# Kernel optimization log

Hardware: AMD Instinct MI355X
Metric: run time of the kernel (lower is better)

Reference implementation:

```python
import jax, jax.numpy as jnp
import numpy as np

N_COL, N_CON, E = 100000, 20000, 800000
D_COL, D_CON, H = 16, 8, 128


def _segment_mean(msgs, dst_idx, n_dst):
    # sum then divide by in-degree (0-degree nodes get 0, matching PyG scatter-mean)
    s = jax.ops.segment_sum(msgs, dst_idx, num_segments=n_dst)
    cnt = jax.ops.segment_sum(jnp.ones((dst_idx.shape[0], 1), msgs.dtype), dst_idx, num_segments=n_dst)
    return s / jnp.maximum(cnt, 1.0)


def _sage(x_src, x_dst, src_idx, dst_idx, Wl, bl, Wr):
    # PyG SAGEConv(mean): lin_l(mean_j x_j) + lin_r(x_i); lin_r has no bias
    agg = _segment_mean(x_src[src_idx], dst_idx, x_dst.shape[0])
    return agg @ Wl.T + bl + x_dst @ Wr.T


def setup_inputs():
    key = jax.random.key(0)
    ks = jax.random.split(key, 24)
    rn = lambda k, shape, s=0.05: jax.random.normal(k, shape, jnp.float32) * s
    z = lambda shape: jnp.zeros(shape, jnp.float32)
    inp = {
        'x_col': jax.random.normal(ks[0], (N_COL, D_COL), jnp.float32),
        'x_con': jax.random.normal(ks[1], (N_CON, D_CON), jnp.float32),
        'edge_col': jax.random.randint(ks[2], (E,), 0, N_COL, jnp.int32),
        'edge_con': jax.random.randint(ks[3], (E,), 0, N_CON, jnp.int32),
        'W_col': rn(ks[4], (H, D_COL)), 'b_col': z((H,)),
        'W_con': rn(ks[5], (H, D_CON)), 'b_con': z((H,)),
        'c1_cn_Wl': rn(ks[6], (H, H)), 'c1_cn_bl': z((H,)), 'c1_cn_Wr': rn(ks[7], (H, H)),
        'c1_nc_Wl': rn(ks[8], (H, H)), 'c1_nc_bl': z((H,)), 'c1_nc_Wr': rn(ks[9], (H, H)),
        'c2_cn_Wl': rn(ks[10], (H, H)), 'c2_cn_bl': z((H,)), 'c2_cn_Wr': rn(ks[11], (H, H)),
        'c2_nc_Wl': rn(ks[12], (H, H)), 'c2_nc_bl': z((H,)), 'c2_nc_Wr': rn(ks[13], (H, H)),
        'q_W1': rn(ks[14], (H // 2, H)), 'q_b1': z((H // 2,)),
        'q_W2': rn(ks[15], (1, H // 2)), 'q_b2': z((1,)),
    }
    return inp


def reference(x_col, x_con, edge_col, edge_con,
              W_col, b_col, W_con, b_con,
              c1_cn_Wl, c1_cn_bl, c1_cn_Wr, c1_nc_Wl, c1_nc_bl, c1_nc_Wr,
              c2_cn_Wl, c2_cn_bl, c2_cn_Wr, c2_nc_Wl, c2_nc_bl, c2_nc_Wr,
              q_W1, q_b1, q_W2, q_b2):
    relu = jax.nn.relu
    h_col = relu(x_col @ W_col.T + b_col)  # [N_COL, H]
    h_con = relu(x_con @ W_con.T + b_con)  # [N_CON, H]
    # conv1: 'serves' col->con, 'served_by' con->col (reverse edges)
    n_con = relu(_sage(h_col, h_con, edge_col, edge_con, c1_cn_Wl, c1_cn_bl, c1_cn_Wr))
    n_col = relu(_sage(h_con, h_col, edge_con, edge_col, c1_nc_Wl, c1_nc_bl, c1_nc_Wr))
    # conv2
    h_con2 = relu(_sage(n_col, n_con, edge_col, edge_con, c2_cn_Wl, c2_cn_bl, c2_cn_Wr))
    h_col2 = relu(_sage(n_con, n_col, edge_con, edge_col, c2_nc_Wl, c2_nc_bl, c2_nc_Wr))
    del h_con2  # constraint embeddings unused for Q-head
    q = relu(h_col2 @ q_W1.T + q_b1) @ q_W2.T + q_b2  # [N_COL, 1]
    return q[:, 0]
```

## Files before the change

### kernel.cpp

```cpp
#include <hip/hip_runtime.h>

#define N_COL 100000
#define N_CON 20000
#define HDIM 128
#define SCAN_B 1024

__global__ void transpose_k(const float* __restrict__ src, float* __restrict__ dst, int R, int C) {
    int idx = blockIdx.x * blockDim.x + threadIdx.x;
    if (idx < R * C) {
        int r = idx / C, c = idx - r * C;
        dst[c * R + r] = src[idx];
    }
}

template <int D>
__global__ __launch_bounds__(256) void encoder_k(const float* __restrict__ x,
                                                 const float* __restrict__ WT,
                                                 const float* __restrict__ b,
                                                 float* __restrict__ out, int N) {
    int idx = blockIdx.x * blockDim.x + threadIdx.x;
    if (idx >= N * HDIM) return;
    int n = idx >> 7, h = idx & 127;
    const float* xr = x + (size_t)n * D;
    float acc = b[h];
#pragma unroll
    for (int k = 0; k < D; k++) acc = fmaf(xr[k], WT[k * HDIM + h], acc);
    out[idx] = fmaxf(acc, 0.f);
}

__global__ void count_k(const int* __restrict__ ecol, const int* __restrict__ econ,
                        int* cnt_col, int* cnt_con, int E) {
    int e = blockIdx.x * blockDim.x + threadIdx.x;
    if (e < E) {
        atomicAdd(&cnt_col[ecol[e]], 1);
        atomicAdd(&cnt_con[econ[e]], 1);
    }
}

__global__ __launch_bounds__(256) void scan1_k(const int* __restrict__ cnt, int n,
                                               int* __restrict__ offs, int* __restrict__ partials) {
    __shared__ int lds[256];
    int t = threadIdx.x;
    int base = blockIdx.x * SCAN_B + t * 4;
    int v[4], s = 0;
#pragma unroll
    for (int i = 0; i < 4; i++) { int idx = base + i; v[i] = (idx < n) ? cnt[idx] : 0; s += v[i]; }
    lds[t] = s; __syncthreads();
    for (int off = 1; off < 256; off <<= 1) {
        int x = (t >= off) ? lds[t - off] : 0; __syncthreads();
        lds[t] += x; __syncthreads();
    }
    int excl = lds[t] - s;
    if (t == 255) partials[blockIdx.x] = lds[255];
    int run = excl;
#pragma unroll
    for (int i = 0; i < 4; i++) { int idx = base + i; if (idx < n) offs[idx] = run; run += v[i]; }
}

__global__ __launch_bounds__(256) void scan2_k(int* partials, int nb) {
    __shared__ int lds[256];
    int t = threadIdx.x;
    int v = (t < nb) ? partials[t] : 0;
    lds[t] = v; __syncthreads();
    for (int off = 1; off < 256; off <<= 1) {
        int x = (t >= off) ? lds[t - off] : 0; __syncthreads();
        lds[t] += x; __syncthreads();
    }
    if (t < nb) partials[t] = lds[t] - v;
}

__global__ void scan3_k(int* offs, int n, const int* __restrict__ partials) {
    int i = blockIdx.x * blockDim.x + threadIdx.x;
    if (i < n) offs[i] += partials[i / SCAN_B];
}

__global__ void fill_k(const int* __restrict__ sidx, const int* __restrict__ didx,
                       const int* __restrict__ offs, int* cursor, int* __restrict__ srclist, int E) {
    int e = blockIdx.x * blockDim.x + threadIdx.x;
    if (e < E) {
        int d = didx[e];
        int p = offs[d] + atomicAdd(&cursor[d], 1);
        srclist[p] = sidx[e];
    }
}

__global__ __launch_bounds__(256) void gather_mean_k(const float* __restrict__ tab,
                                                     const int* __restrict__ srclist,
                                                     const int* __restrict__ offs,
                                                     const int* __restrict__ cnt,
                                                     float* __restrict__ out, int N) {
    int wid = threadIdx.x >> 6, lane = threadIdx.x & 63;
    int n = blockIdx.x * 4 + wid;
    if (n >= N) return;
    int c = cnt[n], st = offs[n];
    const int* sl = srclist + st;
    int half = lane >> 5, q = (lane & 31) * 4;
    float ax = 0.f, ay = 0.f, az = 0.f, aw = 0.f;
    int j = 0;
    for (; j + 1 < c; j += 2) {
        int s = sl[j + half];
        float4 a = *reinterpret_cast<const float4*>(tab + (size_t)s * HDIM + q);
        ax += a.x; ay += a.y; az += a.z; aw += a.w;
    }
    if (j < c && half == 0) {
        int s = sl[j];
        float4 a = *reinterpret_cast<const float4*>(tab + (size_t)s * HDIM + q);
        ax += a.x; ay += a.y; az += a.z; aw += a.w;
    }
    ax += __shfl_xor(ax, 32); ay += __shfl_xor(ay, 32);
    az += __shfl_xor(az, 32); aw += __shfl_xor(aw, 32);
    if (half == 0) {
        float inv = 1.f / fmaxf((float)c, 1.f);
        float4 r; r.x = ax * inv; r.y = ay * inv; r.z = az * inv; r.w = aw * inv;
        *reinterpret_cast<float4*>(out + (size_t)n * HDIM + q) = r;
    }
}

__global__ __launch_bounds__(256) void gather_dual_k(const float* __restrict__ t1,
                                                     const float* __restrict__ t2,
                                                     const int* __restrict__ srclist,
                                                     const int* __restrict__ offs,
                                                     const int* __restrict__ cnt,
                                                     float* __restrict__ o1,
                                                     float* __restrict__ o2, int N) {
    int wid = threadIdx.x >> 6, lane = threadIdx.x & 63;
    int n = blockIdx.x * 4 + wid;
    if (n >= N) return;
    int c = cnt[n], st = offs[n];
    const int* sl = srclist + st;
    int half = lane >> 5, q = (lane & 31) * 4;
    const float* tab = half ? t2 : t1;
    float ax = 0.f, ay = 0.f, az = 0.f, aw = 0.f;
    int j = 0;
    for (; j + 1 < c; j += 2) {
        int s0 = sl[j], s1 = sl[j + 1];
        float4 a = *reinterpret_cast<const float4*>(tab + (size_t)s0 * HDIM + q);
        float4 b = *reinterpret_cast<const float4*>(tab + (size_t)s1 * HDIM + q);
        ax += a.x + b.x; ay += a.y + b.y; az += a.z + b.z; aw += a.w + b.w;
    }
    if (j < c) {
        int s0 = sl[j];
        float4 a = *reinterpret_cast<const float4*>(tab + (size_t)s0 * HDIM + q);
        ax += a.x; ay += a.y; az += a.z; aw += a.w;
    }
    float inv = 1.f / fmaxf((float)c, 1.f);
    float4 r; r.x = ax * inv; r.y = ay * inv; r.z = az * inv; r.w = aw * inv;
    float* op = (half ? o2 : o1) + (size_t)n * HDIM + q;
    *reinterpret_cast<float4*>(op) = r;
}

__device__ __forceinline__ void gemm_core(float (*As)[36], float (*Ws)[132],
                                          const float* __restrict__ src,
                                          const float* __restrict__ W,
                                          int n0, int N, int t, float acc[4][8]) {
    int tx = t & 15, ty = t >> 4;
    int ar = t >> 2, akq = (t & 3) * 8;
    int wk = t >> 3, wc = (t & 7) * 16;
    for (int kb = 0; kb < 4; ++kb) {
        int k0 = kb * 32;
        {
            int row = n0 + ar;
            float4 v0 = make_float4(0.f, 0.f, 0.f, 0.f), v1 = v0;
            if (row < N) {
                const float* ap = src + (size_t)row * HDIM + k0 + akq;
                v0 = *reinterpret_cast<const float4*>(ap);
                v1 = *reinterpret_cast<const float4*>(ap + 4);
            }
            *reinterpret_cast<float4*>(&As[ar][akq]) = v0;
            *reinterpret_cast<float4*>(&As[ar][akq + 4]) = v1;
        }
        {
            const float* wp = W + (size_t)(k0 + wk) * HDIM + wc;
#pragma unroll
            for (int jj = 0; jj < 4; jj++)
                *reinterpret_cast<float4*>(&Ws[wk][wc + 4 * jj]) =
                    *reinterpret_cast<const float4*>(wp + 4 * jj);
        }
        __syncthreads();
#pragma unroll
        for (int k4 = 0; k4 < 8; ++k4) {
            float4 av[4];
#pragma unroll
            for (int i = 0; i < 4; i++)
                av[i] = *reinterpret_cast<const float4*>(&As[ty * 4 + i][k4 * 4]);
#pragma unroll
            for (int kk = 0; kk < 4; kk++) {
                float4 w0 = *reinterpret_cast<const float4*>(&Ws[k4 * 4 + kk][tx * 4]);
                float4 w1 = *reinterpret_cast<const float4*>(&Ws[k4 * 4 + kk][64 + tx * 4]);
                float w[8] = {w0.x, w0.y, w0.z, w0.w, w1.x, w1.y, w1.z, w1.w};
#pragma unroll
                for (int i = 0; i < 4; i++) {
                    float avk = (kk == 0) ? av[i].x : (kk == 1) ? av[i].y
                                : (kk == 2) ? av[i].z : av[i].w;
#pragma unroll
                    for (int j = 0; j < 8; j++) acc[i][j] = fmaf(avk, w[j], acc[i][j]);
                }
            }
        }
        __syncthreads();
    }
}

__device__ __forceinline__ void gemm_core_h(float (*Ha)[132], float (*Ws)[132],
                                            const float* __restrict__ W,
                                            int t, float acc[4][8]) {
    int tx = t & 15, ty = t >> 4;
    int wk = t >> 3, wc = (t & 7) * 16;
    for (int kb = 0; kb < 4; ++kb) {
        int k0 = kb * 32;
        {
            const float* wp = W + (size_t)(k0 + wk) * HDIM + wc;
#pragma unroll
            for (int jj = 0; jj < 4; jj++)
                *reinterpret_cast<float4*>(&Ws[wk][wc + 4 * jj]) =
                    *reinterpret_cast<const float4*>(wp + 4 * jj);
        }
        __syncthreads();
#pragma unroll
        for (int k4 = 0; k4 < 8; ++k4) {
            float4 av[4];
#pragma unroll
            for (int i = 0; i < 4; i++)
                av[i] = *reinterpret_cast<const float4*>(&Ha[ty * 4 + i][k0 + k4 * 4]);
#pragma unroll
            for (int kk = 0; kk < 4; kk++) {
                float4 w0 = *reinterpret_cast<const float4*>(&Ws[k4 * 4 + kk][tx * 4]);
                float4 w1 = *reinterpret_cast<const float4*>(&Ws[k4 * 4 + kk][64 + tx * 4]);
                float w[8] = {w0.x, w0.y, w0.z, w0.w, w1.x, w1.y, w1.z, w1.w};
#pragma unroll
                for (int i = 0; i < 4; i++) {
                    float avk = (kk == 0) ? av[i].x : (kk == 1) ? av[i].y
                                : (kk == 2) ? av[i].z : av[i].w;
#pragma unroll
                    for (int j = 0; j < 8; j++) acc[i][j] = fmaf(avk, w[j], acc[i][j]);
                }
            }
        }
        __syncthreads();
    }
}

__global__ __launch_bounds__(256) void lin_k(const float* __restrict__ src,
                                             const float* __restrict__ WT,
                                             float* __restrict__ out, int N) {
    __shared__ __align__(16) float As[64][36];
    __shared__ __align__(16) float Ws[32][132];
    int t = threadIdx.x;
    int tx = t & 15, ty = t >> 4;
    int n0 = blockIdx.x * 64;
    float acc[4][8];
#pragma unroll
    for (int i = 0; i < 4; i++)
#pragma unroll
        for (int j = 0; j < 8; j++) acc[i][j] = 0.f;
    gemm_core(As, Ws, src, WT, n0, N, t, acc);
#pragma unroll
    for (int i = 0; i < 4; i++) {
        int row = n0 + ty * 4 + i;
        if (row < N) {
            float* op = out + (size_t)row * HDIM;
            *reinterpret_cast<float4*>(op + tx * 4) = make_float4(acc[i][0], acc[i][1], acc[i][2], acc[i][3]);
            *reinterpret_cast<float4*>(op + 64 + tx * 4) = make_float4(acc[i][4], acc[i][5], acc[i][6], acc[i][7]);
        }
    }
}

__global__ __launch_bounds__(256) void sage_gemm_k(const float* __restrict__ agg,
                                                   const float* __restrict__ xdst,
                                                   const float* __restrict__ WlT,
                                                   const float* __restrict__ bl,
                                                   const float* __restrict__ WrT,
                                                   float* __restrict__ out, int N) {
    __shared__ __align__(16) float As[64][36];
    __shared__ __align__(16) float Ws[32][132];
    int t = threadIdx.x;
    int tx = t & 15, ty = t >> 4;
    int n0 = blockIdx.x * 64;
    float acc[4][8];
#pragma unroll
    for (int i = 0; i < 4; i++)
#pragma unroll
        for (int j = 0; j < 8; j++) acc[i][j] = 0.f;
    gemm_core(As, Ws, agg, WlT, n0, N, t, acc);
    gemm_core(As, Ws, xdst, WrT, n0, N, t, acc);
    float4 b0 = *reinterpret_cast<const float4*>(bl + tx * 4);
    float4 b1 = *reinterpret_cast<const float4*>(bl + 64 + tx * 4);
    float bb[8] = {b0.x, b0.y, b0.z, b0.w, b1.x, b1.y, b1.z, b1.w};
#pragma unroll
    for (int i = 0; i < 4; i++) {
        int row = n0 + ty * 4 + i;
        if (row < N) {
            float4 r0, r1;
            r0.x = fmaxf(acc[i][0] + bb[0], 0.f);
            r0.y = fmaxf(acc[i][1] + bb[1], 0.f);
            r0.z = fmaxf(acc[i][2] + bb[2], 0.f);
            r0.w = fmaxf(acc[i][3] + bb[3], 0.f);
            r1.x = fmaxf(acc[i][4] + bb[4], 0.f);
            r1.y = fmaxf(acc[i][5] + bb[5], 0.f);
            r1.z = fmaxf(acc[i][6] + bb[6], 0.f);
            r1.w = fmaxf(acc[i][7] + bb[7], 0.f);
            float* op = out + (size_t)row * HDIM;
            *reinterpret_cast<float4*>(op + tx * 4) = r0;
            *reinterpret_cast<float4*>(op + 64 + tx * 4) = r1;
        }
    }
}

__global__ __launch_bounds__(256) void col_mega_k(const float* __restrict__ c0_1,
                                                  const float* __restrict__ c0_2,
                                                  const float* __restrict__ xdst,
                                                  const float* __restrict__ Wr1T,
                                                  const float* __restrict__ bl1,
                                                  const float* __restrict__ Wr2T,
                                                  const float* __restrict__ bl2,
                                                  const float* __restrict__ W1T,
                                                  const float* __restrict__ b1v,
                                                  const float* __restrict__ W2,
                                                  const float* __restrict__ b2,
                                                  float* __restrict__ out, int N) {
    __shared__ __align__(16) char smem[50688];
    float (*H)[132] = reinterpret_cast<float(*)[132]>(smem);
    float (*Ws)[132] = reinterpret_cast<float(*)[132]>(smem + 33792);
    int t = threadIdx.x;
    int tx = t & 15, ty = t >> 4;
    int n0 = blockIdx.x * 64;

    {
        int xr = t >> 2, xc0 = (t & 3) * 32;
        int row = n0 + xr;
        if (row < N) {
            const float* xp = xdst + (size_t)row * HDIM + xc0;
#pragma unroll
            for (int jj = 0; jj < 8; jj++)
                *reinterpret_cast<float4*>(&H[xr][xc0 + 4 * jj]) =
                    *reinterpret_cast<const float4*>(xp + 4 * jj);
        } else {
            float4 z = make_float4(0.f, 0.f, 0.f, 0.f);
#pragma unroll
            for (int jj = 0; jj < 8; jj++)
                *reinterpret_cast<float4*>(&H[xr][xc0 + 4 * jj]) = z;
        }
    }
    float acc[4][8];
#pragma unroll
    for (int i = 0; i < 4; i++)
#pragma unroll
        for (int j = 0; j < 8; j++) acc[i][j] = 0.f;
    gemm_core_h(H, Ws, Wr1T, t, acc);
    {
        float4 b0 = *reinterpret_cast<const float4*>(bl1 + tx * 4);
        float4 b1 = *reinterpret_cast<const float4*>(bl1 + 64 + tx * 4);
        float bb[8] = {b0.x, b0.y, b0.z, b0.w, b1.x, b1.y, b1.z, b1.w};
#pragma unroll
        for (int i = 0; i < 4; i++) {
            int row = n0 + ty * 4 + i;
            float4 ca = make_float4(0.f, 0.f, 0.f, 0.f), cb = ca;
            if (row < N) {
                const float* cp = c0_1 + (size_t)row * HDIM;
                ca = *reinterpret_cast<const float4*>(cp + tx * 4);
                cb = *reinterpret_cast<const float4*>(cp + 64 + tx * 4);
            }
            float* hp = &H[ty * 4 + i][0];
            *reinterpret_cast<float4*>(hp + tx * 4) = make_float4(
                fmaxf(acc[i][0] + ca.x + bb[0], 0.f), fmaxf(acc[i][1] + ca.y + bb[1], 0.f),
                fmaxf(acc[i][2] + ca.z + bb[2], 0.f), fmaxf(acc[i][3] + ca.w + bb[3], 0.f));
            *reinterpret_cast<float4*>(hp + 64 + tx * 4) = make_float4(
                fmaxf(acc[i][4] + cb.x + bb[4], 0.f), fmaxf(acc[i][5] + cb.y + bb[5], 0.f),
                fmaxf(acc[i][6] + cb.z + bb[6], 0.f), fmaxf(acc[i][7] + cb.w + bb[7], 0.f));
        }
    }
#pragma unroll
    for (int i = 0; i < 4; i++)
#pragma unroll
        for (int j = 0; j < 8; j++) acc[i][j] = 0.f;
    gemm_core_h(H, Ws, Wr2T, t, acc);
    {
        float4 b0 = *reinterpret_cast<const float4*>(bl2 + tx * 4);
        float4 b1 = *reinterpret_cast<const float4*>(bl2 + 64 + tx * 4);
        float bb[8] = {b0.x, b0.y, b0.z, b0.w, b1.x, b1.y, b1.z, b1.w};
#pragma unroll
        for (int i = 0; i < 4; i++) {
            int row = n0 + ty * 4 + i;
            float4 ca = make_float4(0.f, 0.f, 0.f, 0.f), cb = ca;
            if (row < N) {
                const float* cp = c0_2 + (size_t)row * HDIM;
                ca = *reinterpret_cast<const float4*>(cp + tx * 4);
                cb = *reinterpret_cast<const float4*>(cp + 64 + tx * 4);
            }
            float* hp = &H[ty * 4 + i][0];
            *reinterpret_cast<float4*>(hp + tx * 4) = make_float4(
                fmaxf(acc[i][0] + ca.x + bb[0], 0.f), fmaxf(acc[i][1] + ca.y + bb[1], 0.f),
                fmaxf(acc[i][2] + ca.z + bb[2], 0.f), fmaxf(acc[i][3] + ca.w + bb[3], 0.f));
            *reinterpret_cast<float4*>(hp + 64 + tx * 4) = make_float4(
                fmaxf(acc[i][4] + cb.x + bb[4], 0.f), fmaxf(acc[i][5] + cb.y + bb[5], 0.f),
                fmaxf(acc[i][6] + cb.z + bb[6], 0.f), fmaxf(acc[i][7] + cb.w + bb[7], 0.f));
        }
    }
    __syncthreads();

    int tx2 = t & 7, ty2 = t >> 3;
    float acc2[2][8];
#pragma unroll
    for (int i = 0; i < 2; i++)
#pragma unroll
        for (int j = 0; j < 8; j++) acc2[i][j] = 0.f;
    for (int k4 = 0; k4 < HDIM / 4; ++k4) {
        float4 a0 = *reinterpret_cast<const float4*>(&H[ty2 * 2 + 0][k4 * 4]);
        float4 a1 = *reinterpret_cast<const float4*>(&H[ty2 * 2 + 1][k4 * 4]);
        float a[2][4] = {{a0.x, a0.y, a0.z, a0.w}, {a1.x, a1.y, a1.z, a1.w}};
#pragma unroll
        for (int kk = 0; kk < 4; kk++) {
            const float* wp = W1T + (size_t)(k4 * 4 + kk) * 64 + tx2 * 8;
            float4 w0 = *reinterpret_cast<const float4*>(wp);
            float4 w1 = *reinterpret_cast<const float4*>(wp + 4);
            float w[8] = {w0.x, w0.y, w0.z, w0.w, w1.x, w1.y, w1.z, w1.w};
#pragma unroll
            for (int i = 0; i < 2; i++)
#pragma unroll
                for (int j = 0; j < 8; j++) acc2[i][j] = fmaf(a[i][kk], w[j], acc2[i][j]);
        }
    }
    {
        float4 c0v = *reinterpret_cast<const float4*>(b1v + tx2 * 8);
        float4 c1v = *reinterpret_cast<const float4*>(b1v + tx2 * 8 + 4);
        float bb1[8] = {c0v.x, c0v.y, c0v.z, c0v.w, c1v.x, c1v.y, c1v.z, c1v.w};
        float4 d0 = *reinterpret_cast<const float4*>(W2 + tx2 * 8);
        float4 d1 = *reinterpret_cast<const float4*>(W2 + tx2 * 8 + 4);
        float w2[8] = {d0.x, d0.y, d0.z, d0.w, d1.x, d1.y, d1.z, d1.w};
#pragma unroll
        for (int i = 0; i < 2; i++) {
            float v = 0.f;
#pragma unroll
            for (int j = 0; j < 8; j++) v = fmaf(fmaxf(acc2[i][j] + bb1[j], 0.f), w2[j], v);
            v += __shfl_xor(v, 1);
            v += __shfl_xor(v, 2);
            v += __shfl_xor(v, 4);
            int row = n0 + ty2 * 2 + i;
            if (tx2 == 0 && row < N) out[row] = v + b2[0];
        }
    }
}

extern "C" void kernel_launch(void* const* d_in, const int* in_sizes, int n_in,
                              void* d_out, int out_size, void* d_ws, size_t ws_size,
                              hipStream_t stream) {
    const float* x_col = (const float*)d_in[0];
    const float* x_con = (const float*)d_in[1];
    const int* edge_col = (const int*)d_in[2];
    const int* edge_con = (const int*)d_in[3];
    const float* W_col = (const float*)d_in[4];
    const float* b_col = (const float*)d_in[5];
    const float* W_con = (const float*)d_in[6];
    const float* b_con = (const float*)d_in[7];
    const float* c1_cn_Wl = (const float*)d_in[8];
    const float* c1_cn_bl = (const float*)d_in[9];
    const float* c1_cn_Wr = (const float*)d_in[10];
    const float* c1_nc_Wl = (const float*)d_in[11];
    const float* c1_nc_bl = (const float*)d_in[12];
    const float* c1_nc_Wr = (const float*)d_in[13];
    const float* c2_nc_Wl = (const float*)d_in[17];
    const float* c2_nc_bl = (const float*)d_in[18];
    const float* c2_nc_Wr = (const float*)d_in[19];
    const float* q_W1 = (const float*)d_in[20];
    const float* q_b1 = (const float*)d_in[21];
    const float* q_W2 = (const float*)d_in[22];
    const float* q_b2 = (const float*)d_in[23];
    float* out = (float*)d_out;
    const int E = in_sizes[2];

    float* ws = (float*)d_ws;
    size_t o = 0;
    float* h_col = ws + o;   o += (size_t)N_COL * HDIM;
    float* h_con = ws + o;   o += (size_t)N_CON * HDIM;
    float* n_con = ws + o;   o += (size_t)N_CON * HDIM;
    float* c01 = ws + o;     o += (size_t)N_COL * HDIM;
    float* c02 = ws + o;     o += (size_t)N_COL * HDIM;
    float* buf1 = ws + o;    o += (size_t)N_CON * HDIM;
    float* W_colT = ws + o;  o += 16 * HDIM;
    float* W_conT = ws + o;  o += 8 * HDIM;
    float* c1_cn_WlT = ws + o; o += HDIM * HDIM;
    float* c1_cn_WrT = ws + o; o += HDIM * HDIM;
    float* c1_nc_WlT = ws + o; o += HDIM * HDIM;
    float* c1_nc_WrT = ws + o; o += HDIM * HDIM;
    float* c2_nc_WlT = ws + o; o += HDIM * HDIM;
    float* c2_nc_WrT = ws + o; o += HDIM * HDIM;
    float* q_W1T = ws + o;     o += HDIM * 64;
    int* iws = (int*)(ws + o);
    size_t io = 0;
    int* cnt_col = iws + io;  io += N_COL;
    int* cnt_con = iws + io;  io += N_CON;
    int* offs_col = iws + io; io += N_COL;
    int* offs_con = iws + io; io += N_CON;
    int* cursor = iws + io;   io += N_COL;
    int* partials = iws + io; io += 256;
    int* srclist_col = iws + io; io += E;
    int* srclist_con = iws + io; io += E;
    float* buf2 = h_con;

    auto T = [&](const float* s, float* d, int R, int C) {
        transpose_k<<<(R * C + 255) / 256, 256, 0, stream>>>(s, d, R, C);
    };
    T(W_col, W_colT, HDIM, 16);
    T(W_con, W_conT, HDIM, 8);
    T(c1_cn_Wl, c1_cn_WlT, HDIM, HDIM);
    T(c1_cn_Wr, c1_cn_WrT, HDIM, HDIM);
    T(c1_nc_Wl, c1_nc_WlT, HDIM, HDIM);
    T(c1_nc_Wr, c1_nc_WrT, HDIM, HDIM);
    T(c2_nc_Wl, c2_nc_WlT, HDIM, HDIM);
    T(c2_nc_Wr, c2_nc_WrT, HDIM, HDIM);
    T(q_W1, q_W1T, 64, HDIM);

    encoder_k<16><<<((size_t)N_COL * HDIM + 255) / 256, 256, 0, stream>>>(x_col, W_colT, b_col, h_col, N_COL);
    encoder_k<8><<<((size_t)N_CON * HDIM + 255) / 256, 256, 0, stream>>>(x_con, W_conT, b_con, h_con, N_CON);

    hipMemsetAsync(cnt_col, 0, (N_COL + N_CON) * sizeof(int), stream);
    count_k<<<(E + 255) / 256, 256, 0, stream>>>(edge_col, edge_con, cnt_col, cnt_con, E);

    int nb_col = (N_COL + SCAN_B - 1) / SCAN_B;
    int nb_con = (N_CON + SCAN_B - 1) / SCAN_B;
    scan1_k<<<nb_col, 256, 0, stream>>>(cnt_col, N_COL, offs_col, partials);
    scan2_k<<<1, 256, 0, stream>>>(partials, nb_col);
    scan3_k<<<(N_COL + 255) / 256, 256, 0, stream>>>(offs_col, N_COL, partials);
    scan1_k<<<nb_con, 256, 0, stream>>>(cnt_con, N_CON, offs_con, partials);
    scan2_k<<<1, 256, 0, stream>>>(partials, nb_con);
    scan3_k<<<(N_CON + 255) / 256, 256, 0, stream>>>(offs_con, N_CON, partials);

    hipMemsetAsync(cursor, 0, N_COL * sizeof(int), stream);
    fill_k<<<(E + 255) / 256, 256, 0, stream>>>(edge_con, edge_col, offs_col, cursor, srclist_col, E);
    hipMemsetAsync(cursor, 0, N_CON * sizeof(int), stream);
    fill_k<<<(E + 255) / 256, 256, 0, stream>>>(edge_col, edge_con, offs_con, cursor, srclist_con, E);

    gather_mean_k<<<(N_CON + 3) / 4, 256, 0, stream>>>(h_col, srclist_con, offs_con, cnt_con, buf1, N_CON);
    sage_gemm_k<<<(N_CON + 63) / 64, 256, 0, stream>>>(buf1, h_con, c1_cn_WlT, c1_cn_bl, c1_cn_WrT, n_con, N_CON);

    lin_k<<<(N_CON + 63) / 64, 256, 0, stream>>>(h_con, c1_nc_WlT, buf1, N_CON);
    lin_k<<<(N_CON + 63) / 64, 256, 0, stream>>>(n_con, c2_nc_WlT, buf2, N_CON);
    gather_dual_k<<<(N_COL + 3) / 4, 256, 0, stream>>>(buf1, buf2, srclist_col, offs_col, cnt_col,
                                                       c01, c02, N_COL);

    col_mega_k<<<(N_COL + 63) / 64, 256, 0, stream>>>(c01, c02, h_col,
                                                      c1_nc_WrT, c1_nc_bl, c2_nc_WrT, c2_nc_bl,
                                                      q_W1T, q_b1, q_W2, q_b2, out, N_COL);
}
```

Baseline: 740.5 us.

## Batch graph preprocessing launches, interleave dual-table layout, recompute column encoder in mega kernel

Measured after the change: 708.7 us. 4.3% less time.

```diff
diff --git a/kernel.cpp b/kernel.cpp
--- a/kernel.cpp
+++ b/kernel.cpp
@@ -5,12 +5,30 @@
 #define HDIM 128
 #define SCAN_B 1024
 
-__global__ void transpose_k(const float* __restrict__ src, float* __restrict__ dst, int R, int C) {
-    int idx = blockIdx.x * blockDim.x + threadIdx.x;
-    if (idx < R * C) {
-        int r = idx / C, c = idx - r * C;
-        dst[c * R + r] = src[idx];
-    }
+__global__ __launch_bounds__(256) void prep_k(
+    const float* W_col, float* W_colT, const float* W_con, float* W_conT,
+    const float* a2, float* b2_, const float* a3, float* b3,
+    const float* a4, float* b4, const float* a5, float* b5,
+    const float* a6, float* b6, const float* a7, float* b7,
+    const float* qW1, float* qW1T) {
+    int i = blockIdx.x * blockDim.x + threadIdx.x;
+#define TRANS(SRC, DST, R, C, CNT)                        \
+    if (i < (CNT)) {                                      \
+        int r = i / (C), c = i - r * (C);                 \
+        DST[c * (R) + r] = SRC[i];                        \
+        return;                                           \
+    }                                                     \
+    i -= (CNT);
+    TRANS(W_col, W_colT, 128, 16, 2048)
+    TRANS(W_con, W_conT, 128, 8, 1024)
+    TRANS(a2, b2_, 128, 128, 16384)
+    TRANS(a3, b3, 128, 128, 16384)
+    TRANS(a4, b4, 128, 128, 16384)
+    TRANS(a5, b5, 128, 128, 16384)
+    TRANS(a6, b6, 128, 128, 16384)
+    TRANS(a7, b7, 128, 128, 16384)
+    TRANS(qW1, qW1T, 64, 128, 8192)
+#undef TRANS
 }
 
 template <int D>
@@ -29,11 +47,11 @@
 }
 
 __global__ void count_k(const int* __restrict__ ecol, const int* __restrict__ econ,
-                        int* cnt_col, int* cnt_con, int E) {
+                        int* cnt, int E) {
     int e = blockIdx.x * blockDim.x + threadIdx.x;
     if (e < E) {
-        atomicAdd(&cnt_col[ecol[e]], 1);
-        atomicAdd(&cnt_con[econ[e]], 1);
+        atomicAdd(&cnt[ecol[e]], 1);
+        atomicAdd(&cnt[N_COL + econ[e]], 1);
     }
 }
 
@@ -74,13 +92,15 @@
     if (i < n) offs[i] += partials[i / SCAN_B];
 }
 
-__global__ void fill_k(const int* __restrict__ sidx, const int* __restrict__ didx,
-                       const int* __restrict__ offs, int* cursor, int* __restrict__ srclist, int E) {
+__global__ void fill2_k(const int* __restrict__ ecol, const int* __restrict__ econ,
+                        const int* __restrict__ offs, int* cursor, int* __restrict__ srclist, int E) {
     int e = blockIdx.x * blockDim.x + threadIdx.x;
     if (e < E) {
-        int d = didx[e];
-        int p = offs[d] + atomicAdd(&cursor[d], 1);
-        srclist[p] = sidx[e];
+        int dc = ecol[e], dn = econ[e];
+        int p1 = offs[dc] + atomicAdd(&cursor[dc], 1);
+        srclist[p1] = dn;
+        int p2 = offs[N_COL + dn] + atomicAdd(&cursor[N_COL + dn], 1);
+        srclist[p2] = dc;
     }
 }
 
@@ -116,37 +136,33 @@
     }
 }
 
-__global__ __launch_bounds__(256) void gather_dual_k(const float* __restrict__ t1,
-                                                     const float* __restrict__ t2,
+__global__ __launch_bounds__(256) void gather_dual_k(const float* __restrict__ tabC,
                                                      const int* __restrict__ srclist,
                                                      const int* __restrict__ offs,
                                                      const int* __restrict__ cnt,
-                                                     float* __restrict__ o1,
-                                                     float* __restrict__ o2, int N) {
+                                                     float* __restrict__ c0C, int N) {
     int wid = threadIdx.x >> 6, lane = threadIdx.x & 63;
     int n = blockIdx.x * 4 + wid;
     if (n >= N) return;
     int c = cnt[n], st = offs[n];
     const int* sl = srclist + st;
-    int half = lane >> 5, q = (lane & 31) * 4;
-    const float* tab = half ? t2 : t1;
+    int q = (lane & 63) * 4;
     float ax = 0.f, ay = 0.f, az = 0.f, aw = 0.f;
     int j = 0;
     for (; j + 1 < c; j += 2) {
         int s0 = sl[j], s1 = sl[j + 1];
-        float4 a = *reinterpret_cast<const float4*>(tab + (size_t)s0 * HDIM + q);
-        float4 b = *reinterpret_cast<const float4*>(tab + (size_t)s1 * HDIM + q);
+        float4 a = *reinterpret_cast<const float4*>(tabC + (size_t)s0 * 256 + q);
+        float4 b = *reinterpret_cast<const float4*>(tabC + (size_t)s1 * 256 + q);
         ax += a.x + b.x; ay += a.y + b.y; az += a.z + b.z; aw += a.w + b.w;
     }
     if (j < c) {
         int s0 = sl[j];
-        float4 a = *reinterpret_cast<const float4*>(tab + (size_t)s0 * HDIM + q);
+        float4 a = *reinterpret_cast<const float4*>(tabC + (size_t)s0 * 256 + q);
         ax += a.x; ay += a.y; az += a.z; aw += a.w;
     }
     float inv = 1.f / fmaxf((float)c, 1.f);
     float4 r; r.x = ax * inv; r.y = ay * inv; r.z = az * inv; r.w = aw * inv;
-    float* op = (half ? o2 : o1) + (size_t)n * HDIM + q;
-    *reinterpret_cast<float4*>(op) = r;
+    *reinterpret_cast<float4*>(c0C + (size_t)n * 256 + q) = r;
 }
 
 __device__ __forceinline__ void gemm_core(float (*As)[36], float (*Ws)[132],
@@ -240,25 +256,30 @@
     }
 }
 
-__global__ __launch_bounds__(256) void lin_k(const float* __restrict__ src,
-                                             const float* __restrict__ WT,
-                                             float* __restrict__ out, int N) {
+__global__ __launch_bounds__(256) void lin2_k(const float* __restrict__ s1,
+                                              const float* __restrict__ W1,
+                                              const float* __restrict__ s2,
+                                              const float* __restrict__ W2,
+                                              float* __restrict__ outC, int N) {
     __shared__ __align__(16) float As[64][36];
     __shared__ __align__(16) float Ws[32][132];
     int t = threadIdx.x;
     int tx = t & 15, ty = t >> 4;
     int n0 = blockIdx.x * 64;
+    const float* src = blockIdx.y ? s2 : s1;
+    const float* W = blockIdx.y ? W2 : W1;
+    int coff = blockIdx.y * 128;
     float acc[4][8];
 #pragma unroll
     for (int i = 0; i < 4; i++)
 #pragma unroll
         for (int j = 0; j < 8; j++) acc[i][j] = 0.f;
-    gemm_core(As, Ws, src, WT, n0, N, t, acc);
+    gemm_core(As, Ws, src, W, n0, N, t, acc);
 #pragma unroll
     for (int i = 0; i < 4; i++) {
         int row = n0 + ty * 4 + i;
         if (row < N) {
-            float* op = out + (size_t)row * HDIM;
+            float* op = outC + (size_t)row * 256 + coff;
             *reinterpret_cast<float4*>(op + tx * 4) = make_float4(acc[i][0], acc[i][1], acc[i][2], acc[i][3]);
             *reinterpret_cast<float4*>(op + 64 + tx * 4) = make_float4(acc[i][4], acc[i][5], acc[i][6], acc[i][7]);
         }
@@ -306,9 +327,10 @@
     }
 }
 
-__global__ __launch_bounds__(256) void col_mega_k(const float* __restrict__ c0_1,
-                                                  const float* __restrict__ c0_2,
-                                                  const float* __restrict__ xdst,
+__global__ __launch_bounds__(256) void col_mega_k(const float* __restrict__ c0C,
+                                                  const float* __restrict__ xcol,
+                                                  const float* __restrict__ WcT,
+                                                  const float* __restrict__ bcol,
                                                   const float* __restrict__ Wr1T,
                                                   const float* __restrict__ bl1,
                                                   const float* __restrict__ Wr2T,
@@ -321,27 +343,58 @@
     __shared__ __align__(16) char smem[50688];
     float (*H)[132] = reinterpret_cast<float(*)[132]>(smem);
     float (*Ws)[132] = reinterpret_cast<float(*)[132]>(smem + 33792);
+    float (*Xs)[20] = reinterpret_cast<float(*)[20]>(smem + 33792);
+    float (*Wc)[132] = reinterpret_cast<float(*)[132]>(smem + 33792 + 5120);
     int t = threadIdx.x;
     int tx = t & 15, ty = t >> 4;
     int n0 = blockIdx.x * 64;
+    float acc[4][8];
 
     {
-        int xr = t >> 2, xc0 = (t & 3) * 32;
+        int xr = t >> 2, xq = (t & 3) * 4;
         int row = n0 + xr;
-        if (row < N) {
-            const float* xp = xdst + (size_t)row * HDIM + xc0;
-#pragma unroll
-            for (int jj = 0; jj < 8; jj++)
-                *reinterpret_cast<float4*>(&H[xr][xc0 + 4 * jj]) =
-                    *reinterpret_cast<const float4*>(xp + 4 * jj);
-        } else {
-            float4 z = make_float4(0.f, 0.f, 0.f, 0.f);
-#pragma unroll
-            for (int jj = 0; jj < 8; jj++)
-                *reinterpret_cast<float4*>(&H[xr][xc0 + 4 * jj]) = z;
-        }
-    }
-    float acc[4][8];
+        float4 xv = make_float4(0.f, 0.f, 0.f, 0.f);
+        if (row < N) xv = *reinterpret_cast<const float4*>(xcol + (size_t)row * 16 + xq);
+        *reinterpret_cast<float4*>(&Xs[xr][xq]) = xv;
+        const float* wp = WcT + (t >> 4) * HDIM + (t & 15) * 8;
+        *reinterpret_cast<float4*>(&Wc[t >> 4][(t & 15) * 8]) = *reinterpret_cast<const float4*>(wp);
+        *reinterpret_cast<float4*>(&Wc[t >> 4][(t & 15) * 8 + 4]) = *reinterpret_cast<const float4*>(wp + 4);
+    }
+    __syncthreads();
+#pragma unroll
+    for (int i = 0; i < 4; i++)
+#pragma unroll
+        for (int j = 0; j < 8; j++) acc[i][j] = 0.f;
+#pragma unroll
+    for (int k = 0; k < 16; ++k) {
+        float a[4];
+#pragma unroll
+        for (int i = 0; i < 4; i++) a[i] = Xs[ty * 4 + i][k];
+        float4 w0 = *reinterpret_cast<const float4*>(&Wc[k][tx * 4]);
+        float4 w1 = *reinterpret_cast<const float4*>(&Wc[k][64 + tx * 4]);
+        float w[8] = {w0.x, w0.y, w0.z, w0.w, w1.x, w1.y, w1.z, w1.w};
+#pragma unroll
+        for (int i = 0; i < 4; i++)
+#pragma unroll
+            for (int j = 0; j < 8; j++) acc[i][j] = fmaf(a[i], w[j], acc[i][j]);
+    }
+    __syncthreads();
+    {
+        float4 b0 = *reinterpret_cast<const float4*>(bcol + tx * 4);
+        float4 b1 = *reinterpret_cast<const float4*>(bcol + 64 + tx * 4);
+#pragma unroll
+        for (int i = 0; i < 4; i++) {
+            float* hp = &H[ty * 4 + i][0];
+            *reinterpret_cast<float4*>(hp + tx * 4) = make_float4(
+                fmaxf(acc[i][0] + b0.x, 0.f), fmaxf(acc[i][1] + b0.y, 0.f),
+                fmaxf(acc[i][2] + b0.z, 0.f), fmaxf(acc[i][3] + b0.w, 0.f));
+            *reinterpret_cast<float4*>(hp + 64 + tx * 4) = make_float4(
+                fmaxf(acc[i][4] + b1.x, 0.f), fmaxf(acc[i][5] + b1.y, 0.f),
+                fmaxf(acc[i][6] + b1.z, 0.f), fmaxf(acc[i][7] + b1.w, 0.f));
+        }
+    }
+    __syncthreads();
+
 #pragma unroll
     for (int i = 0; i < 4; i++)
 #pragma unroll
@@ -350,25 +403,25 @@
     {
         float4 b0 = *reinterpret_cast<const float4*>(bl1 + tx * 4);
         float4 b1 = *reinterpret_cast<const float4*>(bl1 + 64 + tx * 4);
-        float bb[8] = {b0.x, b0.y, b0.z, b0.w, b1.x, b1.y, b1.z, b1.w};
 #pragma unroll
         for (int i = 0; i < 4; i++) {
             int row = n0 + ty * 4 + i;
             float4 ca = make_float4(0.f, 0.f, 0.f, 0.f), cb = ca;
             if (row < N) {
-                const float* cp = c0_1 + (size_t)row * HDIM;
+                const float* cp = c0C + (size_t)row * 256;
                 ca = *reinterpret_cast<const float4*>(cp + tx * 4);
                 cb = *reinterpret_cast<const float4*>(cp + 64 + tx * 4);
             }
             float* hp = &H[ty * 4 + i][0];
             *reinterpret_cast<float4*>(hp + tx * 4) = make_float4(
-                fmaxf(acc[i][0] + ca.x + bb[0], 0.f), fmaxf(acc[i][1] + ca.y + bb[1], 0.f),
-                fmaxf(acc[i][2] + ca.z + bb[2], 0.f), fmaxf(acc[i][3] + ca.w + bb[3], 0.f));
+                fmaxf(acc[i][0] + ca.x + b0.x, 0.f), fmaxf(acc[i][1] + ca.y + b0.y, 0.f),
+                fmaxf(acc[i][2] + ca.z + b0.z, 0.f), fmaxf(acc[i][3] + ca.w + b0.w, 0.f));
             *reinterpret_cast<float4*>(hp + 64 + tx * 4) = make_float4(
-                fmaxf(acc[i][4] + cb.x + bb[4], 0.f), fmaxf(acc[i][5] + cb.y + bb[5], 0.f),
-                fmaxf(acc[i][6] + cb.z + bb[6], 0.f), fmaxf(acc[i][7] + cb.w + bb[7], 0.f));
-        }
-    }
+                fmaxf(acc[i][4] + cb.x + b1.x, 0.f), fmaxf(acc[i][5] + cb.y + b1.y, 0.f),
+                fmaxf(acc[i][6] + cb.z + b1.z, 0.f), fmaxf(acc[i][7] + cb.w + b1.w, 0.f));
+        }
+    }
+
 #pragma unroll
     for (int i = 0; i < 4; i++)
 #pragma unroll
@@ -377,23 +430,22 @@
     {
         float4 b0 = *reinterpret_cast<const float4*>(bl2 + tx * 4);
         float4 b1 = *reinterpret_cast<const float4*>(bl2 + 64 + tx * 4);
-        float bb[8] = {b0.x, b0.y, b0.z, b0.w, b1.x, b1.y, b1.z, b1.w};
 #pragma unroll
         for (int i = 0; i < 4; i++) {
             int row = n0 + ty * 4 + i;
             float4 ca = make_float4(0.f, 0.f, 0.f, 0.f), cb = ca;
             if (row < N) {
-                const float* cp = c0_2 + (size_t)row * HDIM;
+                const float* cp = c0C + (size_t)row * 256 + 128;
                 ca = *reinterpret_cast<const float4*>(cp + tx * 4);
                 cb = *reinterpret_cast<const float4*>(cp + 64 + tx * 4);
             }
             float* hp = &H[ty * 4 + i][0];
             *reinterpret_cast<float4*>(hp + tx * 4) = make_float4(
-                fmaxf(acc[i][0] + ca.x + bb[0], 0.f), fmaxf(acc[i][1] + ca.y + bb[1], 0.f),
-                fmaxf(acc[i][2] + ca.z + bb[2], 0.f), fmaxf(acc[i][3] + ca.w + bb[3], 0.f));
+                fmaxf(acc[i][0] + ca.x + b0.x, 0.f), fmaxf(acc[i][1] + ca.y + b0.y, 0.f),
+                fmaxf(acc[i][2] + ca.z + b0.z, 0.f), fmaxf(acc[i][3] + ca.w + b0.w, 0.f));
             *reinterpret_cast<float4*>(hp + 64 + tx * 4) = make_float4(
-                fmaxf(acc[i][4] + cb.x + bb[4], 0.f), fmaxf(acc[i][5] + cb.y + bb[5], 0.f),
-                fmaxf(acc[i][6] + cb.z + bb[6], 0.f), fmaxf(acc[i][7] + cb.w + bb[7], 0.f));
+                fmaxf(acc[i][4] + cb.x + b1.x, 0.f), fmaxf(acc[i][5] + cb.y + b1.y, 0.f),
+                fmaxf(acc[i][6] + cb.z + b1.z, 0.f), fmaxf(acc[i][7] + cb.w + b1.w, 0.f));
         }
     }
     __syncthreads();
@@ -473,8 +525,8 @@
     float* h_col = ws + o;   o += (size_t)N_COL * HDIM;
     float* h_con = ws + o;   o += (size_t)N_CON * HDIM;
     float* n_con = ws + o;   o += (size_t)N_CON * HDIM;
-    float* c01 = ws + o;     o += (size_t)N_COL * HDIM;
-    float* c02 = ws + o;     o += (size_t)N_COL * HDIM;
+    float* c0C = ws + o;     o += (size_t)N_COL * 256;
+    float* linC = ws + o;    o += (size_t)N_CON * 256;
     float* buf1 = ws + o;    o += (size_t)N_CON * HDIM;
     float* W_colT = ws + o;  o += 16 * HDIM;
     float* W_conT = ws + o;  o += 8 * HDIM;
@@ -487,58 +539,39 @@
     float* q_W1T = ws + o;     o += HDIM * 64;
     int* iws = (int*)(ws + o);
     size_t io = 0;
-    int* cnt_col = iws + io;  io += N_COL;
-    int* cnt_con = iws + io;  io += N_CON;
-    int* offs_col = iws + io; io += N_COL;
-    int* offs_con = iws + io; io += N_CON;
-    int* cursor = iws + io;   io += N_COL;
+    int* cnt = iws + io;     io += N_COL + N_CON;
+    int* cursor = iws + io;  io += N_COL + N_CON;
+    int* offs = iws + io;    io += N_COL + N_CON;
     int* partials = iws + io; io += 256;
-    int* srclist_col = iws + io; io += E;
-    int* srclist_con = iws + io; io += E;
-    float* buf2 = h_con;
-
-    auto T = [&](const float* s, float* d, int R, int C) {
-        transpose_k<<<(R * C + 255) / 256, 256, 0, stream>>>(s, d, R, C);
-    };
-    T(W_col, W_colT, HDIM, 16);
-    T(W_con, W_conT, HDIM, 8);
-    T(c1_cn_Wl, c1_cn_WlT, HDIM, HDIM);
-    T(c1_cn_Wr, c1_cn_WrT, HDIM, HDIM);
-    T(c1_nc_Wl, c1_nc_WlT, HDIM, HDIM);
-    T(c1_nc_Wr, c1_nc_WrT, HDIM, HDIM);
-    T(c2_nc_Wl, c2_nc_WlT, HDIM, HDIM);
-    T(c2_nc_Wr, c2_nc_WrT, HDIM, HDIM);
-    T(q_W1, q_W1T, 64, HDIM);
+    int* srclist = iws + io; io += 2 * (size_t)E;
+    const int NTOT = N_COL + N_CON;
+
+    prep_k<<<(109568 + 255) / 256, 256, 0, stream>>>(
+        W_col, W_colT, W_con, W_conT,
+        c1_cn_Wl, c1_cn_WlT, c1_cn_Wr, c1_cn_WrT,
+        c1_nc_Wl, c1_nc_WlT, c1_nc_Wr, c1_nc_WrT,
+        c2_nc_Wl, c2_nc_WlT, c2_nc_Wr, c2_nc_WrT,
+        q_W1, q_W1T);
 
     encoder_k<16><<<((size_t)N_COL * HDIM + 255) / 256, 256, 0, stream>>>(x_col, W_colT, b_col, h_col, N_COL);
     encoder_k<8><<<((size_t)N_CON * HDIM + 255) / 256, 256, 0, stream>>>(x_con, W_conT, b_con, h_con, N_CON);
 
-    hipMemsetAsync(cnt_col, 0, (N_COL + N_CON) * sizeof(int), stream);
-    count_k<<<(E + 255) / 256, 256, 0, stream>>>(edge_col, edge_con, cnt_col, cnt_con, E);
-
-    int nb_col = (N_COL + SCAN_B - 1) / SCAN_B;
-    int nb_con = (N_CON + SCAN_B - 1) / SCAN_B;
-    scan1_k<<<nb_col, 256, 0, stream>>>(cnt_col, N_COL, offs_col, partials);
-    scan2_k<<<1, 256, 0, stream>>>(partials, nb_col);
-    scan3_k<<<(N_COL + 255) / 256, 256, 0, stream>>>(offs_col, N_COL, partials);
-    scan1_k<<<nb_con, 256, 0, stream>>>(cnt_con, N_CON, offs_con, partials);
-    scan2_k<<<1, 256, 0, stream>>>(partials, nb_con);
-    scan3_k<<<(N_CON + 255) / 256, 256, 0, stream>>>(offs_con, N_CON, partials);
-
-    hipMemsetAsync(cursor, 0, N_COL * sizeof(int), stream);
-    fill_k<<<(E + 255) / 256, 256, 0, stream>>>(edge_con, edge_col, offs_col, cursor, srclist_col, E);
-    hipMemsetAsync(cursor, 0, N_CON * sizeof(int), stream);
-    fill_k<<<(E + 255) / 256, 256, 0, stream>>>(edge_col, edge_con, offs_con, cursor, srclist_con, E);
-
-    gather_mean_k<<<(N_CON + 3) / 4, 256, 0, stream>>>(h_col, srclist_con, offs_con, cnt_con, buf1, N_CON);
+    hipMemsetAsync(cnt, 0, 2 * NTOT * sizeof(int), stream);
+    count_k<<<(E + 255) / 256, 256, 0, stream>>>(edge_col, edge_con, cnt, E);
+    int nb = (NTOT + SCAN_B - 1) / SCAN_B;
+    scan1_k<<<nb, 256, 0, stream>>>(cnt, NTOT, offs, partials);
+    scan2_k<<<1, 256, 0, stream>>>(partials, nb);
+    scan3_k<<<(NTOT + 255) / 256, 256, 0, stream>>>(offs, NTOT, partials);
+    fill2_k<<<(E + 255) / 256, 256, 0, stream>>>(edge_col, edge_con, offs, cursor, srclist, E);
+
+    gather_mean_k<<<(N_CON + 3) / 4, 256, 0, stream>>>(h_col, srclist, offs + N_COL, cnt + N_COL, buf1, N_CON);
     sage_gemm_k<<<(N_CON + 63) / 64, 256, 0, stream>>>(buf1, h_con, c1_cn_WlT, c1_cn_bl, c1_cn_WrT, n_con, N_CON);
 
-    lin_k<<<(N_CON + 63) / 64, 256, 0, stream>>>(h_con, c1_nc_WlT, buf1, N_CON);
-    lin_k<<<(N_CON + 63) / 64, 256, 0, stream>>>(n_con, c2_nc_WlT, buf2, N_CON);
-    gather_dual_k<<<(N_COL + 3) / 4, 256, 0, stream>>>(buf1, buf2, srclist_col, offs_col, cnt_col,
-                                                       c01, c02, N_COL);
-
-    col_mega_k<<<(N_COL + 63) / 64, 256, 0, stream>>>(c01, c02, h_col,
+    dim3 lgrid((N_CON + 63) / 64, 2);
+    lin2_k<<<lgrid, 256, 0, stream>>>(h_con, c1_nc_WlT, n_con, c2_nc_WlT, linC, N_CON);
+    gather_dual_k<<<(N_COL + 3) / 4, 256, 0, stream>>>(linC, srclist, offs, cnt, c0C, N_COL);
+
+    col_mega_k<<<(N_COL + 63) / 64, 256, 0, stream>>>(c0C, x_col, W_colT, b_col,
                                                       c1_nc_WrT, c1_nc_bl, c2_nc_WrT, c2_nc_bl,
                                                       q_W1T, q_b1, q_W2, q_b2, out, N_COL);
 }
```
